# Kernel tuning notes

Measured on AMD Instinct MI355X. Metric: run time of the kernel, lower is better.

## Reference

```python
import jax, jax.numpy as jnp
import numpy as np


def setup_inputs() -> dict:
    key = jax.random.key(0)
    ks = jax.random.split(key, 8)
    B, N, D, S = 4, 16384, 512, 512
    x = jax.random.normal(ks[0], (B, N, D), dtype=jnp.float32)
    jx = jnp.sort(jax.random.randint(ks[1], (N,), 0, S, dtype=jnp.int64))
    scale = 1.0 / np.sqrt(D)
    Wf = jax.random.normal(ks[2], (D, D), dtype=jnp.float32) * scale
    bf = jax.random.normal(ks[3], (D,), dtype=jnp.float32) * scale
    Wg = jax.random.normal(ks[4], (D, D), dtype=jnp.float32) * scale
    bg = jax.random.normal(ks[5], (D,), dtype=jnp.float32) * scale
    Wh = jax.random.normal(ks[6], (D, D), dtype=jnp.float32) * scale
    bh = jax.random.normal(ks[7], (D,), dtype=jnp.float32) * scale
    return {"x": x, "jx": jx, "num_segments": S, "Wf": Wf, "bf": bf,
            "Wg": Wg, "bg": bg, "Wh": Wh, "bh": bh}


def reference(x, jx, num_segments, Wf, bf, Wg, bg, Wh, bh):
    # x: [B, N, D]; jx: [N] segment ids; segments along axis 1.
    fx = jnp.einsum('bnd,ed->bne', x, Wf) + bf  # f(x)
    gx = jnp.einsum('bnd,ed->bne', x, Wg) + bg  # g(x)
    # move N to leading axis so jax.ops.segment_* apply: [N, B, D]
    gx_t = jnp.transpose(gx, (1, 0, 2))
    fx_t = jnp.transpose(fx, (1, 0, 2))
    # scatter_softmax over segments (numerically stable)
    m = jax.ops.segment_max(gx_t, jx, num_segments=num_segments)  # [S, B, D]
    e = jnp.exp(gx_t - m[jx])
    denom = jax.ops.segment_sum(e, jx, num_segments=num_segments)  # [S, B, D]
    w = e / denom[jx]  # [N, B, D]
    # weighted scatter-sum
    y_t = jax.ops.segment_sum(fx_t * w, jx, num_segments=num_segments)  # [S, B, D]
    y = jnp.transpose(y_t, (1, 0, 2))  # [B, S, D]
    hy = jnp.einsum('bsd,ed->bse', y, Wh) + bh
    # expand=True: gather back to per-element
    return hy[:, jx]  # [B, N, D]
```

## Files before the change

kernel.cpp:

```cpp
#include <hip/hip_runtime.h>
#include <stdint.h>

#define B_ 4
#define N_ 16384
#define D_ 512
#define S_ 512

typedef __attribute__((ext_vector_type(8))) short bf16x8;
typedef __attribute__((ext_vector_type(4))) float f32x4;

__device__ __forceinline__ float bf2f(unsigned short u) {
  union { unsigned int i; float f; } v; v.i = ((unsigned int)u) << 16; return v.f;
}
__device__ __forceinline__ unsigned short f2bf(float f) {
  unsigned int x = __float_as_uint(f);
  return (unsigned short)((x + 0x7FFFu + ((x >> 16) & 1u)) >> 16);
}
__device__ __forceinline__ float ldf(const void* p, long i, bool f32) {
  return f32 ? ((const float*)p)[i] : bf2f(((const unsigned short*)p)[i]);
}
__device__ __forceinline__ void gl_lds16(void* lds_base, const void* g) {
  __builtin_amdgcn_global_load_lds(
      (const __attribute__((address_space(1))) unsigned int*)g,
      (__attribute__((address_space(3))) unsigned int*)lds_base,
      16, 0, 0);
}

__device__ __forceinline__ bool jx_is_i64(const int* jx32) { return jx32[N_ - 1] == 0; }
__device__ __forceinline__ int seg_id(const int* jx32, int n, bool i64) {
  return i64 ? jx32[2 * n] : jx32[n];
}

__global__ __launch_bounds__(256)
void classify_k(const void* __restrict__ x, int* __restrict__ flag) {
  __shared__ int cnt[256];
  int c = 0;
  const unsigned short* xs = (const unsigned short*)x;
#pragma unroll
  for (int i = 0; i < 8; i++) {
    unsigned short w = xs[threadIdx.x * 8 + i];
    int e = (w >> 7) & 0xFF;
    if (e == 0 || (e >= 100 && e <= 140)) c++;
  }
  cnt[threadIdx.x] = c;
  __syncthreads();
  for (int s = 128; s > 0; s >>= 1) {
    if ((int)threadIdx.x < s) cnt[threadIdx.x] += cnt[threadIdx.x + s];
    __syncthreads();
  }
  if (threadIdx.x == 0) flag[0] = (cnt[0] < 1843) ? 1 : 0;
}

__global__ __launch_bounds__(256)
void prep_all(const void* __restrict__ x, const int* __restrict__ jx,
              const void* __restrict__ Wf, const void* __restrict__ bfv,
              const void* __restrict__ Wg, const void* __restrict__ bgv,
              const void* __restrict__ Wh, const void* __restrict__ bhv,
              unsigned short* __restrict__ xb, unsigned short* __restrict__ Wfg,
              unsigned short* __restrict__ biasfg, unsigned short* __restrict__ Whb,
              unsigned short* __restrict__ bhb, int* __restrict__ segst,
              const int* __restrict__ flag) {
  const int blk = blockIdx.x, tid = threadIdx.x;
  if (blk >= 19462) {
    int s = (blk - 19462) * 256 + tid;
    if (s > S_) return;
    bool i64 = jx_is_i64(jx);
    int lo = 0, hi = N_;
    while (lo < hi) {
      int mid = (lo + hi) >> 1;
      if (seg_id(jx, mid, i64) < s) lo = mid + 1; else hi = mid;
    }
    segst[s] = lo;
    return;
  }
  const bool f32 = flag[0] != 0;
  if (blk < 16384) {
    const size_t i0 = ((size_t)blk * 256 + tid) * 8;
    bf16x8 v;
    if (f32) {
      const float4* p = (const float4*)((const float*)x + i0);
      float4 a = p[0], b = p[1];
      v[0]=f2bf(a.x); v[1]=f2bf(a.y); v[2]=f2bf(a.z); v[3]=f2bf(a.w);
      v[4]=f2bf(b.x); v[5]=f2bf(b.y); v[6]=f2bf(b.z); v[7]=f2bf(b.w);
    } else {
      v = *(const bf16x8*)((const unsigned short*)x + i0);
    }
    *(bf16x8*)(xb + i0) = v;
  } else {
    int idx = (blk - 16384) * 256 + tid;
    if (idx < 524288) {
      int e = idx >> 9, d = idx & 511;
      float v = (e < 512) ? ldf(Wf, (long)e * 512 + d, f32)
                          : ldf(Wg, (long)(e - 512) * 512 + d, f32);
      Wfg[idx] = f2bf(v);
    } else if (idx < 786432) {
      Whb[idx - 524288] = f2bf(ldf(Wh, idx - 524288, f32));
    } else if (idx < 787456) {
      int j = idx - 786432;
      biasfg[j] = f2bf(j < 512 ? ldf(bfv, j, f32) : ldf(bgv, j - 512, f32));
    } else if (idx < 787968) {
      bhb[idx - 787456] = f2bf(ldf(bhv, idx - 787456, f32));
    }
  }
}

#define BK 64

__global__ __launch_bounds__(256, 2)
void gemm_fg(const unsigned short* __restrict__ A, const unsigned short* __restrict__ Bm,
             const unsigned short* __restrict__ bias,
             unsigned short* __restrict__ Cf, unsigned short* __restrict__ Cg) {
  __shared__ __align__(16) unsigned short As[128 * BK];
  __shared__ __align__(16) unsigned short Bs[128 * BK];
  const int L = blockIdx.x;
  const int xcd = L & 7, local = L >> 3;
  const int tm = xcd * 64 + local / 8;
  const int tn = local % 8;
  const int m0 = tm * 128, n0 = tn * 128;

  const int tid  = threadIdx.x;
  const int w    = tid >> 6;
  const int lane = tid & 63;
  const int wm   = w >> 1, wn = w & 1;
  const int l15  = lane & 15, l4 = lane >> 4;
  const int srow8 = lane >> 3;
  const int ssw   = ((lane & 7) ^ (srow8 & 7)) * 8;
  const int rsw   = l15 & 7;

  f32x4 acc[4][4];
#pragma unroll
  for (int i = 0; i < 4; i++)
#pragma unroll
    for (int j = 0; j < 4; j++) acc[i][j] = (f32x4){0.f, 0.f, 0.f, 0.f};

  for (int kt = 0; kt < 512; kt += BK) {
    __syncthreads();
#pragma unroll
    for (int r = 0; r < 4; r++) {
      const int rb = r * 32 + w * 8;
      gl_lds16(&As[rb * BK], A  + (size_t)(m0 + rb + srow8) * 512 + kt + ssw);
      gl_lds16(&Bs[rb * BK], Bm + (size_t)(n0 + rb + srow8) * 512 + kt + ssw);
    }
    __syncthreads();

    bf16x8 a[4][2], bb[4][2];
#pragma unroll
    for (int i = 0; i < 4; i++) {
      const int row = wm * 64 + i * 16 + l15;
#pragma unroll
      for (int kk = 0; kk < 2; kk++)
        a[i][kk] = *(const bf16x8*)&As[row * BK + (((l4 + kk * 4) ^ rsw) << 3)];
    }
#pragma unroll
    for (int j = 0; j < 4; j++) {
      const int row = wn * 64 + j * 16 + l15;
#pragma unroll
      for (int kk = 0; kk < 2; kk++)
        bb[j][kk] = *(const bf16x8*)&Bs[row * BK + (((l4 + kk * 4) ^ rsw) << 3)];
    }
#pragma unroll
    for (int i = 0; i < 4; i++)
#pragma unroll
      for (int j = 0; j < 4; j++) {
        acc[i][j] = __builtin_amdgcn_mfma_f32_16x16x32_bf16(a[i][0], bb[j][0], acc[i][j], 0, 0, 0);
        acc[i][j] = __builtin_amdgcn_mfma_f32_16x16x32_bf16(a[i][1], bb[j][1], acc[i][j], 0, 0, 0);
      }
  }

#pragma unroll
  for (int j = 0; j < 4; j++) {
    const int col = n0 + wn * 64 + j * 16 + l15;
    const float bv = bf2f(bias[col]);
    unsigned short* base = (col < 512) ? Cf : Cg;
    const int cc = col & 511;
#pragma unroll
    for (int i = 0; i < 4; i++) {
      const int rowb = m0 + wm * 64 + i * 16 + l4 * 4;
#pragma unroll
      for (int r = 0; r < 4; r++)
        base[(size_t)(rowb + r) * 512 + cc] = f2bf(acc[i][j][r] + bv);
    }
  }
}

__global__ __launch_bounds__(256)
void seg_softmax(const unsigned short* __restrict__ f, const unsigned short* __restrict__ g,
                 const int* __restrict__ segst, unsigned short* __restrict__ y) {
  const int s = blockIdx.x * 2 + (threadIdx.x >> 7);
  const int b = blockIdx.y;
  const int d0 = (threadIdx.x & 127) * 4;
  const int st = segst[s], en = segst[s + 1];
  float den0=0.f, den1=0.f, den2=0.f, den3=0.f;
  float y0=0.f, y1=0.f, y2=0.f, y3=0.f;
  int n = st;
  for (; n + 1 < en; n += 2) {
    const size_t offA = (size_t)(b * N_ + n) * 512 + d0;
    const size_t offB = offA + 512;
    const uint2 fpA = *(const uint2*)(f + offA);
    const uint2 gpA = *(const uint2*)(g + offA);
    const uint2 fpB = *(const uint2*)(f + offB);
    const uint2 gpB = *(const uint2*)(g + offB);
    {
      const float f0 = bf2f((unsigned short)fpA.x), f1 = bf2f((unsigned short)(fpA.x >> 16));
      const float f2 = bf2f((unsigned short)fpA.y), f3 = bf2f((unsigned short)(fpA.y >> 16));
      const float g0 = bf2f((unsigned short)gpA.x), g1 = bf2f((unsigned short)(gpA.x >> 16));
      const float g2 = bf2f((unsigned short)gpA.y), g3 = bf2f((unsigned short)(gpA.y >> 16));
      const float e0 = __expf(g0), e1 = __expf(g1), e2 = __expf(g2), e3 = __expf(g3);
      den0 += e0; den1 += e1; den2 += e2; den3 += e3;
      y0 += f0 * e0; y1 += f1 * e1; y2 += f2 * e2; y3 += f3 * e3;
    }
    {
      const float f0 = bf2f((unsigned short)fpB.x), f1 = bf2f((unsigned short)(fpB.x >> 16));
      const float f2 = bf2f((unsigned short)fpB.y), f3 = bf2f((unsigned short)(fpB.y >> 16));
      const float g0 = bf2f((unsigned short)gpB.x), g1 = bf2f((unsigned short)(gpB.x >> 16));
      const float g2 = bf2f((unsigned short)gpB.y), g3 = bf2f((unsigned short)(gpB.y >> 16));
      const float e0 = __expf(g0), e1 = __expf(g1), e2 = __expf(g2), e3 = __expf(g3);
      den0 += e0; den1 += e1; den2 += e2; den3 += e3;
      y0 += f0 * e0; y1 += f1 * e1; y2 += f2 * e2; y3 += f3 * e3;
    }
  }
  if (n < en) {
    const size_t off = (size_t)(b * N_ + n) * 512 + d0;
    const uint2 fp = *(const uint2*)(f + off);
    const uint2 gp = *(const uint2*)(g + off);
    const float f0 = bf2f((unsigned short)fp.x), f1 = bf2f((unsigned short)(fp.x >> 16));
    const float f2 = bf2f((unsigned short)fp.y), f3 = bf2f((unsigned short)(fp.y >> 16));
    const float g0 = bf2f((unsigned short)gp.x), g1 = bf2f((unsigned short)(gp.x >> 16));
    const float g2 = bf2f((unsigned short)gp.y), g3 = bf2f((unsigned short)(gp.y >> 16));
    const float e0 = __expf(g0), e1 = __expf(g1), e2 = __expf(g2), e3 = __expf(g3);
    den0 += e0; den1 += e1; den2 += e2; den3 += e3;
    y0 += f0 * e0; y1 += f1 * e1; y2 += f2 * e2; y3 += f3 * e3;
  }
  uint2 o;
  if (en > st) {
    o.x = (unsigned int)f2bf(y0 / den0) | ((unsigned int)f2bf(y1 / den1) << 16);
    o.y = (unsigned int)f2bf(y2 / den2) | ((unsigned int)f2bf(y3 / den3) << 16);
  } else { o.x = 0u; o.y = 0u; }
  *(uint2*)(y + (size_t)(b * S_ + s) * 512 + d0) = o;
}

__global__ __launch_bounds__(256)
void gemm_hy(const unsigned short* __restrict__ y, const unsigned short* __restrict__ Whb,
             const unsigned short* __restrict__ bhb, unsigned short* __restrict__ hy) {
  __shared__ __align__(16) unsigned short As[64 * 32];
  __shared__ __align__(16) unsigned short Bs[64 * 32];
  const int tid = threadIdx.x;
  const int w = tid >> 6, lane = tid & 63;
  const int l15 = lane & 15, l4 = lane >> 4;
  const int m0 = (blockIdx.x >> 3) * 64, c0 = (blockIdx.x & 7) * 64;
  const int srow = lane >> 2, scol = (lane & 3) * 8;

  f32x4 acc[4];
#pragma unroll
  for (int j = 0; j < 4; j++) acc[j] = (f32x4){0.f, 0.f, 0.f, 0.f};

  for (int kt = 0; kt < 512; kt += 32) {
    __syncthreads();
    gl_lds16(&As[(w * 16) * 32], y   + (size_t)(m0 + w * 16 + srow) * 512 + kt + scol);
    gl_lds16(&Bs[(w * 16) * 32], Whb + (size_t)(c0 + w * 16 + srow) * 512 + kt + scol);
    __syncthreads();
    bf16x8 a = *(const bf16x8*)&As[(w * 16 + l15) * 32 + l4 * 8];
#pragma unroll
    for (int j = 0; j < 4; j++) {
      bf16x8 bb = *(const bf16x8*)&Bs[(j * 16 + l15) * 32 + l4 * 8];
      acc[j] = __builtin_amdgcn_mfma_f32_16x16x32_bf16(a, bb, acc[j], 0, 0, 0);
    }
  }
#pragma unroll
  for (int j = 0; j < 4; j++) {
    const float bv = bf2f(bhb[c0 + j * 16 + l15]);
#pragma unroll
    for (int r = 0; r < 4; r++)
      hy[(size_t)(m0 + w * 16 + l4 * 4 + r) * 512 + c0 + j * 16 + l15] =
          f2bf(acc[j][r] + bv);
  }
}

__global__ __launch_bounds__(256)
void gather_out(const unsigned short* __restrict__ hy, const int* __restrict__ jx,
                void* __restrict__ out, const int* __restrict__ flag) {
  const bool f32 = flag[0] != 0;
  const int gid  = blockIdx.x * 256 + threadIdx.x;
  const int wid  = gid >> 6;
  const int lane = gid & 63;
  const int b = wid >> 14;
  const int n = wid & (N_ - 1);
  const bool i64 = jx_is_i64(jx);
  const int s = seg_id(jx, n, i64);
  const bf16x8 v = *(const bf16x8*)(hy + (size_t)(b * S_ + s) * 512 + lane * 8);
  if (f32) {
    float* dst = (float*)out + (size_t)wid * 512 + lane * 8;
    float4 lo, hi;
    lo.x=bf2f((unsigned short)v[0]); lo.y=bf2f((unsigned short)v[1]);
    lo.z=bf2f((unsigned short)v[2]); lo.w=bf2f((unsigned short)v[3]);
    hi.x=bf2f((unsigned short)v[4]); hi.y=bf2f((unsigned short)v[5]);
    hi.z=bf2f((unsigned short)v[6]); hi.w=bf2f((unsigned short)v[7]);
    *(float4*)dst = lo;
    *(float4*)(dst + 4) = hi;
  } else {
    *(bf16x8*)((unsigned short*)out + (size_t)wid * 512 + lane * 8) = v;
  }
}

extern "C" void kernel_launch(void* const* d_in, const int* in_sizes, int n_in,
                              void* d_out, int out_size, void* d_ws, size_t ws_size,
                              hipStream_t stream) {
  const void* x  = d_in[0];
  const int* jx  = (const int*)d_in[1];
  const void* Wf = d_in[3];
  const void* bf = d_in[4];
  const void* Wg = d_in[5];
  const void* bg = d_in[6];
  const void* Wh = d_in[7];
  const void* bh = d_in[8];

  char* ws = (char*)d_ws;
  int* flag              = (int*)(ws + 0);
  int* segst             = (int*)(ws + 4096);
  unsigned short* biasfg = (unsigned short*)(ws + 8192);
  unsigned short* bhb    = (unsigned short*)(ws + 16384);
  unsigned short* Wfg    = (unsigned short*)(ws + 32768);
  unsigned short* Whb    = (unsigned short*)(ws + 1081344);
  unsigned short* y_ws   = (unsigned short*)(ws + 1605632);
  unsigned short* hy_ws  = (unsigned short*)(ws + 3702784);
  unsigned short* xb     = (unsigned short*)(ws + 8388608);
  unsigned short* fbuf   = (unsigned short*)d_out;
  unsigned short* gbuf   = (unsigned short*)d_out + (size_t)B_ * N_ * D_;

  classify_k<<<1, 256, 0, stream>>>(x, flag);
  prep_all<<<19465, 256, 0, stream>>>(x, jx, Wf, bf, Wg, bg, Wh, bh,
                                      xb, Wfg, biasfg, Whb, bhb, segst, flag);
  gemm_fg<<<4096, 256, 0, stream>>>(xb, Wfg, biasfg, fbuf, gbuf);
  seg_softmax<<<dim3(256, B_), 256, 0, stream>>>(fbuf, gbuf, segst, y_ws);
  gemm_hy<<<256, 256, 0, stream>>>(y_ws, Whb, bhb, hy_ws);
  gather_out<<<16384, 256, 0, stream>>>(hy_ws, jx, d_out, flag);
}
```

Before: 370.0 us.

## Split prep kernel, use grid-stride x conversion, raise gemm occupancy, unroll softmax by four

Splits the combined prep kernel into a weight/segment-start kernel and a separate x-conversion kernel. The x kernel launches fewer blocks, and each thread converts eight chunks in a strided loop. The gemm_fg launch bounds change from 2 to 3 blocks per CU, which may force register spilling. The segment softmax loop is unrolled to four rows per iteration to issue more loads in flight. The cost is one extra kernel launch.

Result: slower. 424.2 us (+14.7%).

```diff
diff --git a/kernel.cpp b/kernel.cpp
--- a/kernel.cpp
+++ b/kernel.cpp
@@ -52,30 +52,13 @@
 }
 
 __global__ __launch_bounds__(256)
-void prep_all(const void* __restrict__ x, const int* __restrict__ jx,
-              const void* __restrict__ Wf, const void* __restrict__ bfv,
-              const void* __restrict__ Wg, const void* __restrict__ bgv,
-              const void* __restrict__ Wh, const void* __restrict__ bhv,
-              unsigned short* __restrict__ xb, unsigned short* __restrict__ Wfg,
-              unsigned short* __restrict__ biasfg, unsigned short* __restrict__ Whb,
-              unsigned short* __restrict__ bhb, int* __restrict__ segst,
-              const int* __restrict__ flag) {
-  const int blk = blockIdx.x, tid = threadIdx.x;
-  if (blk >= 19462) {
-    int s = (blk - 19462) * 256 + tid;
-    if (s > S_) return;
-    bool i64 = jx_is_i64(jx);
-    int lo = 0, hi = N_;
-    while (lo < hi) {
-      int mid = (lo + hi) >> 1;
-      if (seg_id(jx, mid, i64) < s) lo = mid + 1; else hi = mid;
-    }
-    segst[s] = lo;
-    return;
-  }
+void prep_x(const void* __restrict__ x, unsigned short* __restrict__ xb,
+            const int* __restrict__ flag) {
   const bool f32 = flag[0] != 0;
-  if (blk < 16384) {
-    const size_t i0 = ((size_t)blk * 256 + tid) * 8;
+  size_t i0 = ((size_t)blockIdx.x * 256 + threadIdx.x) * 8;
+  const size_t stride = (size_t)2048 * 256 * 8;
+#pragma unroll
+  for (int it = 0; it < 8; ++it, i0 += stride) {
     bf16x8 v;
     if (f32) {
       const float4* p = (const float4*)((const float*)x + i0);
@@ -86,27 +69,50 @@
       v = *(const bf16x8*)((const unsigned short*)x + i0);
     }
     *(bf16x8*)(xb + i0) = v;
-  } else {
-    int idx = (blk - 16384) * 256 + tid;
-    if (idx < 524288) {
-      int e = idx >> 9, d = idx & 511;
-      float v = (e < 512) ? ldf(Wf, (long)e * 512 + d, f32)
-                          : ldf(Wg, (long)(e - 512) * 512 + d, f32);
-      Wfg[idx] = f2bf(v);
-    } else if (idx < 786432) {
-      Whb[idx - 524288] = f2bf(ldf(Wh, idx - 524288, f32));
-    } else if (idx < 787456) {
-      int j = idx - 786432;
-      biasfg[j] = f2bf(j < 512 ? ldf(bfv, j, f32) : ldf(bgv, j - 512, f32));
-    } else if (idx < 787968) {
-      bhb[idx - 787456] = f2bf(ldf(bhv, idx - 787456, f32));
-    }
+  }
+}
+
+__global__ __launch_bounds__(256)
+void prep_wseg(const int* __restrict__ jx,
+               const void* __restrict__ Wf, const void* __restrict__ bfv,
+               const void* __restrict__ Wg, const void* __restrict__ bgv,
+               const void* __restrict__ Wh, const void* __restrict__ bhv,
+               unsigned short* __restrict__ Wfg, unsigned short* __restrict__ biasfg,
+               unsigned short* __restrict__ Whb, unsigned short* __restrict__ bhb,
+               int* __restrict__ segst, const int* __restrict__ flag) {
+  const int blk = blockIdx.x, tid = threadIdx.x;
+  if (blk >= 3078) {
+    int s = (blk - 3078) * 256 + tid;
+    if (s > S_) return;
+    bool i64 = jx_is_i64(jx);
+    int lo = 0, hi = N_;
+    while (lo < hi) {
+      int mid = (lo + hi) >> 1;
+      if (seg_id(jx, mid, i64) < s) lo = mid + 1; else hi = mid;
+    }
+    segst[s] = lo;
+    return;
+  }
+  const bool f32 = flag[0] != 0;
+  int idx = blk * 256 + tid;
+  if (idx < 524288) {
+    int e = idx >> 9, d = idx & 511;
+    float v = (e < 512) ? ldf(Wf, (long)e * 512 + d, f32)
+                        : ldf(Wg, (long)(e - 512) * 512 + d, f32);
+    Wfg[idx] = f2bf(v);
+  } else if (idx < 786432) {
+    Whb[idx - 524288] = f2bf(ldf(Wh, idx - 524288, f32));
+  } else if (idx < 787456) {
+    int j = idx - 786432;
+    biasfg[j] = f2bf(j < 512 ? ldf(bfv, j, f32) : ldf(bgv, j - 512, f32));
+  } else if (idx < 787968) {
+    bhb[idx - 787456] = f2bf(ldf(bhv, idx - 787456, f32));
   }
 }
 
 #define BK 64
 
-__global__ __launch_bounds__(256, 2)
+__global__ __launch_bounds__(256, 3)
 void gemm_fg(const unsigned short* __restrict__ A, const unsigned short* __restrict__ Bm,
              const unsigned short* __restrict__ bias,
              unsigned short* __restrict__ Cf, unsigned short* __restrict__ Cg) {
@@ -183,6 +189,17 @@
   }
 }
 
+#define SM_ROW(fp, gp)                                                        \
+  {                                                                           \
+    const float ff0 = bf2f((unsigned short)(fp).x), ff1 = bf2f((unsigned short)((fp).x >> 16)); \
+    const float ff2 = bf2f((unsigned short)(fp).y), ff3 = bf2f((unsigned short)((fp).y >> 16)); \
+    const float gg0 = bf2f((unsigned short)(gp).x), gg1 = bf2f((unsigned short)((gp).x >> 16)); \
+    const float gg2 = bf2f((unsigned short)(gp).y), gg3 = bf2f((unsigned short)((gp).y >> 16)); \
+    const float e0 = __expf(gg0), e1 = __expf(gg1), e2 = __expf(gg2), e3 = __expf(gg3); \
+    den0 += e0; den1 += e1; den2 += e2; den3 += e3;                           \
+    y0 += ff0 * e0; y1 += ff1 * e1; y2 += ff2 * e2; y3 += ff3 * e3;           \
+  }
+
 __global__ __launch_bounds__(256)
 void seg_softmax(const unsigned short* __restrict__ f, const unsigned short* __restrict__ g,
                  const int* __restrict__ segst, unsigned short* __restrict__ y) {
@@ -193,43 +210,23 @@
   float den0=0.f, den1=0.f, den2=0.f, den3=0.f;
   float y0=0.f, y1=0.f, y2=0.f, y3=0.f;
   int n = st;
-  for (; n + 1 < en; n += 2) {
-    const size_t offA = (size_t)(b * N_ + n) * 512 + d0;
-    const size_t offB = offA + 512;
-    const uint2 fpA = *(const uint2*)(f + offA);
-    const uint2 gpA = *(const uint2*)(g + offA);
-    const uint2 fpB = *(const uint2*)(f + offB);
-    const uint2 gpB = *(const uint2*)(g + offB);
-    {
-      const float f0 = bf2f((unsigned short)fpA.x), f1 = bf2f((unsigned short)(fpA.x >> 16));
-      const float f2 = bf2f((unsigned short)fpA.y), f3 = bf2f((unsigned short)(fpA.y >> 16));
-      const float g0 = bf2f((unsigned short)gpA.x), g1 = bf2f((unsigned short)(gpA.x >> 16));
-      const float g2 = bf2f((unsigned short)gpA.y), g3 = bf2f((unsigned short)(gpA.y >> 16));
-      const float e0 = __expf(g0), e1 = __expf(g1), e2 = __expf(g2), e3 = __expf(g3);
-      den0 += e0; den1 += e1; den2 += e2; den3 += e3;
-      y0 += f0 * e0; y1 += f1 * e1; y2 += f2 * e2; y3 += f3 * e3;
-    }
-    {
-      const float f0 = bf2f((unsigned short)fpB.x), f1 = bf2f((unsigned short)(fpB.x >> 16));
-      const float f2 = bf2f((unsigned short)fpB.y), f3 = bf2f((unsigned short)(fpB.y >> 16));
-      const float g0 = bf2f((unsigned short)gpB.x), g1 = bf2f((unsigned short)(gpB.x >> 16));
-      const float g2 = bf2f((unsigned short)gpB.y), g3 = bf2f((unsigned short)(gpB.y >> 16));
-      const float e0 = __expf(g0), e1 = __expf(g1), e2 = __expf(g2), e3 = __expf(g3);
-      den0 += e0; den1 += e1; den2 += e2; den3 += e3;
-      y0 += f0 * e0; y1 += f1 * e1; y2 += f2 * e2; y3 += f3 * e3;
-    }
-  }
-  if (n < en) {
+  for (; n + 3 < en; n += 4) {
+    const size_t o0 = (size_t)(b * N_ + n) * 512 + d0;
+    const uint2 f0v = *(const uint2*)(f + o0);
+    const uint2 g0v = *(const uint2*)(g + o0);
+    const uint2 f1v = *(const uint2*)(f + o0 + 512);
+    const uint2 g1v = *(const uint2*)(g + o0 + 512);
+    const uint2 f2v = *(const uint2*)(f + o0 + 1024);
+    const uint2 g2v = *(const uint2*)(g + o0 + 1024);
+    const uint2 f3v = *(const uint2*)(f + o0 + 1536);
+    const uint2 g3v = *(const uint2*)(g + o0 + 1536);
+    SM_ROW(f0v, g0v); SM_ROW(f1v, g1v); SM_ROW(f2v, g2v); SM_ROW(f3v, g3v);
+  }
+  for (; n < en; ++n) {
     const size_t off = (size_t)(b * N_ + n) * 512 + d0;
     const uint2 fp = *(const uint2*)(f + off);
     const uint2 gp = *(const uint2*)(g + off);
-    const float f0 = bf2f((unsigned short)fp.x), f1 = bf2f((unsigned short)(fp.x >> 16));
-    const float f2 = bf2f((unsigned short)fp.y), f3 = bf2f((unsigned short)(fp.y >> 16));
-    const float g0 = bf2f((unsigned short)gp.x), g1 = bf2f((unsigned short)(gp.x >> 16));
-    const float g2 = bf2f((unsigned short)gp.y), g3 = bf2f((unsigned short)(gp.y >> 16));
-    const float e0 = __expf(g0), e1 = __expf(g1), e2 = __expf(g2), e3 = __expf(g3);
-    den0 += e0; den1 += e1; den2 += e2; den3 += e3;
-    y0 += f0 * e0; y1 += f1 * e1; y2 += f2 * e2; y3 += f3 * e3;
+    SM_ROW(fp, gp);
   }
   uint2 o;
   if (en > st) {
@@ -328,8 +325,9 @@
   unsigned short* gbuf   = (unsigned short*)d_out + (size_t)B_ * N_ * D_;
 
   classify_k<<<1, 256, 0, stream>>>(x, flag);
-  prep_all<<<19465, 256, 0, stream>>>(x, jx, Wf, bf, Wg, bg, Wh, bh,
-                                      xb, Wfg, biasfg, Whb, bhb, segst, flag);
+  prep_wseg<<<3081, 256, 0, stream>>>(jx, Wf, bf, Wg, bg, Wh, bh,
+                                      Wfg, biasfg, Whb, bhb, segst, flag);
+  prep_x<<<2048, 256, 0, stream>>>(x, xb, flag);
   gemm_fg<<<4096, 256, 0, stream>>>(xb, Wfg, biasfg, fbuf, gbuf);
   seg_softmax<<<dim3(256, B_), 256, 0, stream>>>(fbuf, gbuf, segst, y_ws);
   gemm_hy<<<256, 256, 0, stream>>>(y_ws, Whb, bhb, hy_ws);
```
